# Performance work log

Measured on AMD Instinct MI355X. Metric: run time of the kernel, lower is better.

Reference implementation:

```python
import jax, jax.numpy as jnp
import numpy as np

N = 100_000      # nodes
E = 1_600_000    # edges (avg degree 16)
D = 32           # feature width (arch = [32, 32, 32])


def setup_inputs() -> dict:
    key = jax.random.key(0)
    ks = jax.random.split(key, 12)
    x = jax.random.normal(ks[0], (N, D), dtype=jnp.float32)
    edge_index = jax.random.randint(ks[1], (2, E), 0, N, dtype=jnp.int32)
    s = 0.1  # weight scale
    inp = {
        "x": x,
        "edge_index": edge_index,
        "W1a": jax.random.normal(ks[2], (D, D), jnp.float32) * s,
        "b1a": jnp.zeros((D,), jnp.float32),
        "W2a": jax.random.normal(ks[3], (D, D), jnp.float32) * s,
        "b2a": jnp.zeros((D,), jnp.float32),
        "W1b": jax.random.normal(ks[4], (D, D), jnp.float32) * s,
        "b1b": jnp.zeros((D,), jnp.float32),
        "W2b": jax.random.normal(ks[5], (D, D), jnp.float32) * s,
        "b2b": jnp.zeros((D,), jnp.float32),
        "op1": 123,
        "op2": 456,
    }
    return inp


def _gcn_layer(x, W, b, src, dst, dis):
    """PyG GCNConv: out = D^{-1/2}(A+I)D^{-1/2} (x W) + b."""
    h = x @ W  # [N, D]
    norm = dis[src] * dis[dst]  # [E]
    agg = jax.ops.segment_sum(h[src] * norm[:, None], dst, num_segments=x.shape[0])
    # self-loop contribution: norm_ii = dis[i]^2
    agg = agg + h * (dis * dis)[:, None]
    return agg + b


def reference(x, edge_index, W1a, b1a, W2a, b2a, W1b, b1b, W2b, b2b, op1, op2):
    src, dst = edge_index[0], edge_index[1]
    # degree at target node, including self-loop (+1)
    deg = jax.ops.segment_sum(jnp.ones((src.shape[0],), x.dtype), dst, num_segments=N) + 1.0
    dis = jax.lax.rsqrt(deg)  # deg^{-1/2}

    def stack(W1, b1, W2, b2):
        h = jax.nn.relu(_gcn_layer(x, W1, b1, src, dst, dis))
        return _gcn_layer(h, W2, b2, src, dst, dis)

    y1 = stack(W1a, b1a, W2a, b2a)  # [N, D]
    y2 = stack(W1b, b1b, W2b, b2b)  # [N, D]
    l1 = jnp.sum(y1[op1] * y1[op2])
    l2 = jnp.sum(y2[op1] * y2[op2])
    return jnp.stack([l1, l2])
```

## Files before the change

### kernel.cpp

```cpp
#include <hip/hip_runtime.h>
#include <hip/hip_bf16.h>

#define DD 32
#define S1CAP 256
#define PERCAP 128
#define E2CAP 1024

__device__ __forceinline__ void s1_insert(int u, int* nidx, int* s1_list, int* cnt) {
    int old = atomicCAS(&nidx[u], 0, -1);
    if (old == 0) {
        int pos = atomicAdd(&cnt[0], 1);
        if (pos < S1CAP) { s1_list[pos] = u; nidx[u] = pos + 1; }
    }
}

__global__ void k_scan1(const int* __restrict__ ei, int E,
                        const int* __restrict__ op1p, const int* __restrict__ op2p,
                        int* __restrict__ nidx, int* __restrict__ s1_list,
                        int* __restrict__ e2_src, int* __restrict__ e2_w,
                        int* __restrict__ cnt) {
    int tid = blockIdx.x * blockDim.x + threadIdx.x;
    int o1 = op1p[0], o2 = op2p[0];
    if (tid == 0) {
        s1_insert(o1, nidx, s1_list, cnt);
        s1_insert(o2, nidx, s1_list, cnt);
    }
    const int* eid = ei + (size_t)E;
    int nchunk = E >> 3;
    if (tid < nchunk) {
        int base = tid * 8;
        int4 a = *reinterpret_cast<const int4*>(eid + base);
        int4 b = *reinterpret_cast<const int4*>(eid + base + 4);
        int dv[8] = {a.x, a.y, a.z, a.w, b.x, b.y, b.z, b.w};
#pragma unroll
        for (int k = 0; k < 8; ++k) {
            int d = dv[k];
            if (d == o1 || d == o2) {
                int s = ei[base + k];
                s1_insert(s, nidx, s1_list, cnt);
                int q = atomicAdd(&cnt[2], 1);
                if (q < E2CAP) { e2_src[q] = s; e2_w[q] = (d == o2); }
            }
        }
    } else if (tid == nchunk) {
        for (int e = nchunk * 8; e < E; ++e) {
            int d = eid[e];
            if (d == o1 || d == o2) {
                int s = ei[e];
                s1_insert(s, nidx, s1_list, cnt);
                int q = atomicAdd(&cnt[2], 1);
                if (q < E2CAP) { e2_src[q] = s; e2_w[q] = (d == o2); }
            }
        }
    }
}

__global__ void k_scan2(const int* __restrict__ ei, int E,
                        const int* __restrict__ nidx,
                        int* __restrict__ e1cnt, int* __restrict__ e1buf,
                        unsigned char* __restrict__ need) {
    int tid = blockIdx.x * blockDim.x + threadIdx.x;
    const int* eid = ei + (size_t)E;
    int nchunk = E >> 3;
    if (tid < nchunk) {
        int base = tid * 8;
        int4 a = *reinterpret_cast<const int4*>(eid + base);
        int4 b = *reinterpret_cast<const int4*>(eid + base + 4);
        int dv[8] = {a.x, a.y, a.z, a.w, b.x, b.y, b.z, b.w};
#pragma unroll
        for (int k = 0; k < 8; ++k) {
            int ix = nidx[dv[k]];
            if (ix > 0) {
                int s = ei[base + k];
                int slot = atomicAdd(&e1cnt[ix - 1], 1);
                if (slot < PERCAP) e1buf[(size_t)(ix - 1) * PERCAP + slot] = s;
                need[s] = 1;
            }
        }
    } else if (tid == nchunk) {
        for (int e = nchunk * 8; e < E; ++e) {
            int ix = nidx[eid[e]];
            if (ix > 0) {
                int s = ei[e];
                int slot = atomicAdd(&e1cnt[ix - 1], 1);
                if (slot < PERCAP) e1buf[(size_t)(ix - 1) * PERCAP + slot] = s;
                need[s] = 1;
            }
        }
    }
}

__global__ void k_scan3(const int* __restrict__ ei, int E,
                        const unsigned char* __restrict__ need,
                        int* __restrict__ deg) {
    int tid = blockIdx.x * blockDim.x + threadIdx.x;
    const int* eid = ei + (size_t)E;
    int nchunk = E >> 3;
    if (tid < nchunk) {
        int base = tid * 8;
        int4 a = *reinterpret_cast<const int4*>(eid + base);
        int4 b = *reinterpret_cast<const int4*>(eid + base + 4);
        int dv[8] = {a.x, a.y, a.z, a.w, b.x, b.y, b.z, b.w};
#pragma unroll
        for (int k = 0; k < 8; ++k) { int d = dv[k]; if (need[d]) atomicAdd(&deg[d], 1); }
    } else if (tid == nchunk) {
        for (int e = nchunk * 8; e < E; ++e) {
            int d = eid[e]; if (need[d]) atomicAdd(&deg[d], 1);
        }
    }
}

__global__ __launch_bounds__(64)
void k_layer1(const float* __restrict__ x, const int* __restrict__ deg,
              const float* __restrict__ W1a, const float* __restrict__ b1a,
              const float* __restrict__ W1b, const float* __restrict__ b1b,
              const int* __restrict__ s1_list, const int* __restrict__ cnt,
              const int* __restrict__ e1cnt, const int* __restrict__ e1buf,
              float* __restrict__ hA, float* __restrict__ hB) {
    __shared__ float Wsh[2][DD][DD];
    __shared__ int   sidx[PERCAP];
    __shared__ float snrm[PERCAP];
    __shared__ float aggsh[DD];
    int s1n = cnt[0] < S1CAP ? cnt[0] : S1CAP;
    int i = blockIdx.x;
    if (i >= s1n) return;
    int t = threadIdx.x, st = t >> 5, dd = t & 31;
    {
        float* w0 = &Wsh[0][0][0];
        float* w1 = &Wsh[1][0][0];
        for (int j = t; j < DD * DD; j += 64) { w0[j] = W1a[j]; w1[j] = W1b[j]; }
    }
    int u = s1_list[i];
    int du = e1cnt[i];
    float dis_u = rsqrtf((float)du + 1.0f);
    int ci = du < PERCAP ? du : PERCAP;
    for (int j = t; j < ci; j += 64) {
        int s = e1buf[(size_t)i * PERCAP + j];
        sidx[j] = s;
        snrm[j] = rsqrtf((float)deg[s] + 1.0f) * dis_u;
    }
    __syncthreads();
    float agg = dis_u * dis_u * x[(size_t)u * DD + dd];
#pragma unroll 4
    for (int j = 0; j < ci; ++j)
        agg += snrm[j] * x[(size_t)sidx[j] * DD + dd];
    if (t < DD) aggsh[dd] = agg;
    __syncthreads();
    float y = st ? b1b[dd] : b1a[dd];
#pragma unroll
    for (int k = 0; k < DD; ++k) y += aggsh[k] * Wsh[st][k][dd];
    y = fmaxf(y, 0.f);
    (st ? hB : hA)[(size_t)i * DD + dd] = y;
}

__global__ __launch_bounds__(128)
void k_layer2(const float* __restrict__ W2a, const float* __restrict__ b2a,
              const float* __restrict__ W2b, const float* __restrict__ b2b,
              const int* __restrict__ op1p, const int* __restrict__ op2p,
              const int* __restrict__ nidx, const int* __restrict__ cnt,
              const int* __restrict__ e1cnt,
              const int* __restrict__ e2_src, const int* __restrict__ e2_w,
              const float* __restrict__ hA, const float* __restrict__ hB,
              float* __restrict__ out) {
    __shared__ float Wsh[2][DD][DD];
    __shared__ int   prow[PERCAP];
    __shared__ int   pw[PERCAP];
    __shared__ float pnrm[PERCAP];
    __shared__ float aggsh[2][2][DD];
    __shared__ float ysh[2][2][DD];
    int t = threadIdx.x;
    int st = t >> 6, w = (t >> 5) & 1, dd = t & 31;
    {
        float* w0 = &Wsh[0][0][0];
        float* w1 = &Wsh[1][0][0];
        for (int j = t; j < DD * DD; j += 128) { w0[j] = W2a[j]; w1[j] = W2b[j]; }
    }
    int o1 = op1p[0], o2 = op2p[0];
    int v = w ? o2 : o1;
    int rv = nidx[v] - 1; if (rv < 0) rv = 0;
    float dis_v = rsqrtf((float)e1cnt[rv] + 1.0f);
    const float* h = st ? hB : hA;
    float agg = dis_v * dis_v * h[(size_t)rv * DD + dd];
    int c2 = cnt[2] < E2CAP ? cnt[2] : E2CAP;
    for (int j0 = 0; j0 < c2; j0 += PERCAP) {
        int jn = c2 - j0; if (jn > PERCAP) jn = PERCAP;
        __syncthreads();
        if (t < jn) {
            int s = e2_src[j0 + t];
            int r = nidx[s] - 1;
            prow[t] = r;
            pw[t]   = e2_w[j0 + t];
            pnrm[t] = (r >= 0) ? rsqrtf((float)e1cnt[r] + 1.0f) : 0.f;
        }
        __syncthreads();
#pragma unroll 4
        for (int j = 0; j < jn; ++j) {
            if (pw[j] == w && prow[j] >= 0)
                agg += (pnrm[j] * dis_v) * h[(size_t)prow[j] * DD + dd];
        }
    }
    aggsh[w][st][dd] = agg;
    __syncthreads();
    float y = st ? b2b[dd] : b2a[dd];
#pragma unroll
    for (int k = 0; k < DD; ++k) y += aggsh[w][st][k] * Wsh[st][k][dd];
    ysh[st][w][dd] = y;
    __syncthreads();
    if (t < 2) {
        float sum = 0.f;
        for (int k = 0; k < DD; ++k) sum += ysh[t][0][k] * ysh[t][1][k];
        out[t] = sum;
    }
}

extern "C" void kernel_launch(void* const* d_in, const int* in_sizes, int n_in,
                              void* d_out, int out_size, void* d_ws, size_t ws_size,
                              hipStream_t stream) {
    const float* x   = (const float*)d_in[0];
    const int*   ei  = (const int*)d_in[1];
    const float* W1a = (const float*)d_in[2];
    const float* b1a = (const float*)d_in[3];
    const float* W2a = (const float*)d_in[4];
    const float* b2a = (const float*)d_in[5];
    const float* W1b = (const float*)d_in[6];
    const float* b1b = (const float*)d_in[7];
    const float* W2b = (const float*)d_in[8];
    const float* b2b = (const float*)d_in[9];
    const int* op1 = (const int*)d_in[10];
    const int* op2 = (const int*)d_in[11];
    int N = in_sizes[0] / DD;
    int E = in_sizes[1] / 2;

    char* p = (char*)d_ws;
    int* cnt   = (int*)p;            p += 64;
    int* e1cnt = (int*)p;            p += S1CAP * 4;
    int* deg   = (int*)p;            p += (size_t)N * 4;
    int* nidx  = (int*)p;            p += (size_t)N * 4;
    unsigned char* need = (unsigned char*)p;
    size_t needpad = ((size_t)N + 15) & ~(size_t)15;
    p += needpad;
    size_t zbytes = 64 + S1CAP * 4 + (size_t)N * 8 + needpad;
    int* s1_list = (int*)p;          p += S1CAP * 4;
    int* e1buf   = (int*)p;          p += (size_t)S1CAP * PERCAP * 4;
    int* e2_src  = (int*)p;          p += E2CAP * 4;
    int* e2_w    = (int*)p;          p += E2CAP * 4;
    float* hA    = (float*)p;        p += (size_t)S1CAP * DD * 4;
    float* hB    = (float*)p;        p += (size_t)S1CAP * DD * 4;

    hipMemsetAsync(d_ws, 0, zbytes, stream);

    int nthreads = (E >> 3) + 1;
    int nb = (nthreads + 255) / 256;
    k_scan1<<<nb, 256, 0, stream>>>(ei, E, op1, op2, nidx, s1_list, e2_src, e2_w, cnt);
    k_scan2<<<nb, 256, 0, stream>>>(ei, E, nidx, e1cnt, e1buf, need);
    k_scan3<<<nb, 256, 0, stream>>>(ei, E, need, deg);
    k_layer1<<<S1CAP, 64, 0, stream>>>(x, deg, W1a, b1a, W1b, b1b,
                                       s1_list, cnt, e1cnt, e1buf, hA, hB);
    k_layer2<<<1, 128, 0, stream>>>(W2a, b2a, W2b, b2b, op1, op2,
                                    nidx, cnt, e1cnt, e2_src, e2_w, hA, hB,
                                    (float*)d_out);
}
```

Before: 128.5 us.

## Fuse layer kernels via last-block-done and reuse e1buf for layer-two edges

Layer 1 and layer 2 are merged into one kernel. The last block to finish, found with an atomic counter and thread fences, runs the final layer-2 reduction, which removes one kernel launch. Layer 2 now reads the op nodes' in-edges from the e1buf lists already built in scan2, so scan1 no longer records e2 edges with a global atomic per match. The layer-1 blocks grow to 128 threads with half idle, and in-edges beyond PERCAP for the op nodes are now truncated.

```diff
diff --git a/kernel.cpp b/kernel.cpp
--- a/kernel.cpp
+++ b/kernel.cpp
@@ -4,7 +4,6 @@
 #define DD 32
 #define S1CAP 256
 #define PERCAP 128
-#define E2CAP 1024
 
 __device__ __forceinline__ void s1_insert(int u, int* nidx, int* s1_list, int* cnt) {
     int old = atomicCAS(&nidx[u], 0, -1);
@@ -17,7 +16,6 @@
 __global__ void k_scan1(const int* __restrict__ ei, int E,
                         const int* __restrict__ op1p, const int* __restrict__ op2p,
                         int* __restrict__ nidx, int* __restrict__ s1_list,
-                        int* __restrict__ e2_src, int* __restrict__ e2_w,
                         int* __restrict__ cnt) {
     int tid = blockIdx.x * blockDim.x + threadIdx.x;
     int o1 = op1p[0], o2 = op2p[0];
@@ -35,22 +33,12 @@
 #pragma unroll
         for (int k = 0; k < 8; ++k) {
             int d = dv[k];
-            if (d == o1 || d == o2) {
-                int s = ei[base + k];
-                s1_insert(s, nidx, s1_list, cnt);
-                int q = atomicAdd(&cnt[2], 1);
-                if (q < E2CAP) { e2_src[q] = s; e2_w[q] = (d == o2); }
-            }
+            if (d == o1 || d == o2) s1_insert(ei[base + k], nidx, s1_list, cnt);
         }
     } else if (tid == nchunk) {
         for (int e = nchunk * 8; e < E; ++e) {
             int d = eid[e];
-            if (d == o1 || d == o2) {
-                int s = ei[e];
-                s1_insert(s, nidx, s1_list, cnt);
-                int q = atomicAdd(&cnt[2], 1);
-                if (q < E2CAP) { e2_src[q] = s; e2_w[q] = (d == o2); }
-            }
+            if (d == o1 || d == o2) s1_insert(ei[e], nidx, s1_list, cnt);
         }
     }
 }
@@ -110,105 +98,118 @@
     }
 }
 
-__global__ __launch_bounds__(64)
-void k_layer1(const float* __restrict__ x, const int* __restrict__ deg,
+__global__ __launch_bounds__(128)
+void k_layers(const float* __restrict__ x, const int* __restrict__ deg,
               const float* __restrict__ W1a, const float* __restrict__ b1a,
               const float* __restrict__ W1b, const float* __restrict__ b1b,
-              const int* __restrict__ s1_list, const int* __restrict__ cnt,
+              const float* __restrict__ W2a, const float* __restrict__ b2a,
+              const float* __restrict__ W2b, const float* __restrict__ b2b,
+              const int* __restrict__ op1p, const int* __restrict__ op2p,
+              const int* __restrict__ nidx, int* __restrict__ cnt,
+              const int* __restrict__ s1_list,
               const int* __restrict__ e1cnt, const int* __restrict__ e1buf,
-              float* __restrict__ hA, float* __restrict__ hB) {
+              float* __restrict__ hA, float* __restrict__ hB,
+              float* __restrict__ out) {
     __shared__ float Wsh[2][DD][DD];
     __shared__ int   sidx[PERCAP];
     __shared__ float snrm[PERCAP];
     __shared__ float aggsh[DD];
+    __shared__ int   prow2[2][PERCAP];
+    __shared__ float pnrm2[2][PERCAP];
+    __shared__ float agg2[2][2][DD];
+    __shared__ float ysh2[2][2][DD];
+    __shared__ int   lastflag;
+
+    int t = threadIdx.x;
+    int i = blockIdx.x;
     int s1n = cnt[0] < S1CAP ? cnt[0] : S1CAP;
-    int i = blockIdx.x;
-    if (i >= s1n) return;
-    int t = threadIdx.x, st = t >> 5, dd = t & 31;
-    {
-        float* w0 = &Wsh[0][0][0];
-        float* w1 = &Wsh[1][0][0];
-        for (int j = t; j < DD * DD; j += 64) { w0[j] = W1a[j]; w1[j] = W1b[j]; }
-    }
-    int u = s1_list[i];
-    int du = e1cnt[i];
-    float dis_u = rsqrtf((float)du + 1.0f);
-    int ci = du < PERCAP ? du : PERCAP;
-    for (int j = t; j < ci; j += 64) {
-        int s = e1buf[(size_t)i * PERCAP + j];
-        sidx[j] = s;
-        snrm[j] = rsqrtf((float)deg[s] + 1.0f) * dis_u;
-    }
-    __syncthreads();
-    float agg = dis_u * dis_u * x[(size_t)u * DD + dd];
+
+    if (i < s1n) {
+        {
+            float* w0 = &Wsh[0][0][0];
+            float* w1 = &Wsh[1][0][0];
+            for (int j = t; j < DD * DD; j += 128) { w0[j] = W1a[j]; w1[j] = W1b[j]; }
+        }
+        int u  = s1_list[i];
+        int du = e1cnt[i];
+        float dis_u = rsqrtf((float)du + 1.0f);
+        int ci = du < PERCAP ? du : PERCAP;
+        for (int j = t; j < ci; j += 128) {
+            int s = e1buf[(size_t)i * PERCAP + j];
+            sidx[j] = s;
+            snrm[j] = rsqrtf((float)deg[s] + 1.0f) * dis_u;
+        }
+        __syncthreads();
+        if (t < 64) {
+            int dd = t & 31;
+            float agg = dis_u * dis_u * x[(size_t)u * DD + dd];
 #pragma unroll 4
-    for (int j = 0; j < ci; ++j)
-        agg += snrm[j] * x[(size_t)sidx[j] * DD + dd];
-    if (t < DD) aggsh[dd] = agg;
-    __syncthreads();
-    float y = st ? b1b[dd] : b1a[dd];
-#pragma unroll
-    for (int k = 0; k < DD; ++k) y += aggsh[k] * Wsh[st][k][dd];
-    y = fmaxf(y, 0.f);
-    (st ? hB : hA)[(size_t)i * DD + dd] = y;
-}
-
-__global__ __launch_bounds__(128)
-void k_layer2(const float* __restrict__ W2a, const float* __restrict__ b2a,
-              const float* __restrict__ W2b, const float* __restrict__ b2b,
-              const int* __restrict__ op1p, const int* __restrict__ op2p,
-              const int* __restrict__ nidx, const int* __restrict__ cnt,
-              const int* __restrict__ e1cnt,
-              const int* __restrict__ e2_src, const int* __restrict__ e2_w,
-              const float* __restrict__ hA, const float* __restrict__ hB,
-              float* __restrict__ out) {
-    __shared__ float Wsh[2][DD][DD];
-    __shared__ int   prow[PERCAP];
-    __shared__ int   pw[PERCAP];
-    __shared__ float pnrm[PERCAP];
-    __shared__ float aggsh[2][2][DD];
-    __shared__ float ysh[2][2][DD];
-    int t = threadIdx.x;
-    int st = t >> 6, w = (t >> 5) & 1, dd = t & 31;
+            for (int j = 0; j < ci; ++j)
+                agg += snrm[j] * x[(size_t)sidx[j] * DD + dd];
+            if (t < DD) aggsh[dd] = agg;
+        }
+        __syncthreads();
+        if (t < 64) {
+            int st = t >> 5, dd = t & 31;
+            float y = st ? b1b[dd] : b1a[dd];
+#pragma unroll
+            for (int k = 0; k < DD; ++k) y += aggsh[k] * Wsh[st][k][dd];
+            y = fmaxf(y, 0.f);
+            (st ? hB : hA)[(size_t)i * DD + dd] = y;
+        }
+    }
+
+    __syncthreads();
+    __threadfence();
+    if (t == 0) lastflag = (atomicAdd(&cnt[3], 1) == (int)gridDim.x - 1);
+    __syncthreads();
+    if (!lastflag) return;
+    __threadfence();
+
     {
         float* w0 = &Wsh[0][0][0];
         float* w1 = &Wsh[1][0][0];
         for (int j = t; j < DD * DD; j += 128) { w0[j] = W2a[j]; w1[j] = W2b[j]; }
     }
     int o1 = op1p[0], o2 = op2p[0];
-    int v = w ? o2 : o1;
-    int rv = nidx[v] - 1; if (rv < 0) rv = 0;
+    int rv0 = nidx[o1] - 1; if (rv0 < 0) rv0 = 0;
+    int rv1 = nidx[o2] - 1; if (rv1 < 0) rv1 = 0;
+    int c0 = e1cnt[rv0]; if (c0 > PERCAP) c0 = PERCAP;
+    int c1 = e1cnt[rv1]; if (c1 > PERCAP) c1 = PERCAP;
+    if (t < c0) {
+        int s = e1buf[(size_t)rv0 * PERCAP + t];
+        int r = nidx[s] - 1;
+        prow2[0][t] = r;
+        pnrm2[0][t] = (r >= 0) ? rsqrtf((float)e1cnt[r] + 1.0f) : 0.f;
+    }
+    if (t < c1) {
+        int s = e1buf[(size_t)rv1 * PERCAP + t];
+        int r = nidx[s] - 1;
+        prow2[1][t] = r;
+        pnrm2[1][t] = (r >= 0) ? rsqrtf((float)e1cnt[r] + 1.0f) : 0.f;
+    }
+    __syncthreads();
+    int st = (t >> 6) & 1, w = (t >> 5) & 1, dd = t & 31;
+    int rv = w ? rv1 : rv0;
+    int cw = w ? c1 : c0;
     float dis_v = rsqrtf((float)e1cnt[rv] + 1.0f);
     const float* h = st ? hB : hA;
     float agg = dis_v * dis_v * h[(size_t)rv * DD + dd];
-    int c2 = cnt[2] < E2CAP ? cnt[2] : E2CAP;
-    for (int j0 = 0; j0 < c2; j0 += PERCAP) {
-        int jn = c2 - j0; if (jn > PERCAP) jn = PERCAP;
-        __syncthreads();
-        if (t < jn) {
-            int s = e2_src[j0 + t];
-            int r = nidx[s] - 1;
-            prow[t] = r;
-            pw[t]   = e2_w[j0 + t];
-            pnrm[t] = (r >= 0) ? rsqrtf((float)e1cnt[r] + 1.0f) : 0.f;
-        }
-        __syncthreads();
 #pragma unroll 4
-        for (int j = 0; j < jn; ++j) {
-            if (pw[j] == w && prow[j] >= 0)
-                agg += (pnrm[j] * dis_v) * h[(size_t)prow[j] * DD + dd];
-        }
-    }
-    aggsh[w][st][dd] = agg;
+    for (int j = 0; j < cw; ++j) {
+        if (prow2[w][j] >= 0)
+            agg += (pnrm2[w][j] * dis_v) * h[(size_t)prow2[w][j] * DD + dd];
+    }
+    agg2[w][st][dd] = agg;
     __syncthreads();
     float y = st ? b2b[dd] : b2a[dd];
 #pragma unroll
-    for (int k = 0; k < DD; ++k) y += aggsh[w][st][k] * Wsh[st][k][dd];
-    ysh[st][w][dd] = y;
+    for (int k = 0; k < DD; ++k) y += agg2[w][st][k] * Wsh[st][k][dd];
+    ysh2[st][w][dd] = y;
     __syncthreads();
     if (t < 2) {
         float sum = 0.f;
-        for (int k = 0; k < DD; ++k) sum += ysh[t][0][k] * ysh[t][1][k];
+        for (int k = 0; k < DD; ++k) sum += ysh2[t][0][k] * ysh2[t][1][k];
         out[t] = sum;
     }
 }
@@ -242,8 +243,6 @@
     size_t zbytes = 64 + S1CAP * 4 + (size_t)N * 8 + needpad;
     int* s1_list = (int*)p;          p += S1CAP * 4;
     int* e1buf   = (int*)p;          p += (size_t)S1CAP * PERCAP * 4;
-    int* e2_src  = (int*)p;          p += E2CAP * 4;
-    int* e2_w    = (int*)p;          p += E2CAP * 4;
     float* hA    = (float*)p;        p += (size_t)S1CAP * DD * 4;
     float* hB    = (float*)p;        p += (size_t)S1CAP * DD * 4;
 
@@ -251,12 +250,11 @@
 
     int nthreads = (E >> 3) + 1;
     int nb = (nthreads + 255) / 256;
-    k_scan1<<<nb, 256, 0, stream>>>(ei, E, op1, op2, nidx, s1_list, e2_src, e2_w, cnt);
+    k_scan1<<<nb, 256, 0, stream>>>(ei, E, op1, op2, nidx, s1_list, cnt);
     k_scan2<<<nb, 256, 0, stream>>>(ei, E, nidx, e1cnt, e1buf, need);
     k_scan3<<<nb, 256, 0, stream>>>(ei, E, need, deg);
-    k_layer1<<<S1CAP, 64, 0, stream>>>(x, deg, W1a, b1a, W1b, b1b,
-                                       s1_list, cnt, e1cnt, e1buf, hA, hB);
-    k_layer2<<<1, 128, 0, stream>>>(W2a, b2a, W2b, b2b, op1, op2,
-                                    nidx, cnt, e1cnt, e2_src, e2_w, hA, hB,
-                                    (float*)d_out);
-}
+    k_layers<<<S1CAP, 128, 0, stream>>>(x, deg, W1a, b1a, W1b, b1b,
+                                        W2a, b2a, W2b, b2b, op1, op2,
+                                        nidx, cnt, s1_list, e1cnt, e1buf,
+                                        hA, hB, (float*)d_out);
+}
```

After: 131.7 us. 2.5% more time.
